# Kernel optimization log

Hardware: AMD Instinct MI355X
Metric: run time of the kernel (lower is better)

Reference implementation:

```python
import jax, jax.numpy as jnp
import numpy as np

B, DIN, N = 8, 256, 2048  # batch, input_dim (orig node_num), attention nodes (orig seq_len)


def setup_inputs() -> dict:
    key = jax.random.key(0)
    k1, k2, k3, k4 = jax.random.split(key, 4)
    x = jax.random.normal(k1, (B, DIN, N), jnp.float32)
    adj = jax.random.randint(k2, (N, N), 0, 2).astype(jnp.int32)  # binary adjacency
    W = jax.random.normal(k3, (DIN, DIN), jnp.float32) * 0.05      # Linear(D, D, bias=False), stored (out, in)
    a = jax.random.normal(k4, (3 * DIN,), jnp.float32) * 0.05      # Linear(3D, 1, bias=False)
    return {"x": x, "adj": adj, "W": W, "a": a}


def reference(x, adj, W, a):
    # x: (B, D, N) -> permute to (B, N, D); attention is over the N axis
    xt = jnp.transpose(x, (0, 2, 1))
    h = xt @ W.T                                   # (B, N, D)
    sim = jnp.einsum('bid,bjd->bij', h, h)         # (B, N, N) pairwise dot products
    n = adj.shape[0]
    # neighbor mask: adj nonzero, diagonal forced off (mask[:, i] = 0 in the loop)
    m = (adj != 0) & (~jnp.eye(n, dtype=bool))
    # context: the torch loop's weighted_h is independent of its k axis, so
    # context[b, k, i, d] == C[b, i, d] = sum_j m[i,j] * sim[b,i,j] * h[b,j,d]
    C = jnp.einsum('bij,bjd->bid', jnp.where(m[None, :, :], sim, 0.0), h)  # (B, N, D)
    d = h.shape[-1]
    a1, a2, a3 = a[:d], a[d:2 * d], a[2 * d:]
    # a([h_i, h_j, C_j]) = a1.h_i + a2.h_j + a3.C_j  (concat never materialized)
    s_i = h @ a1                                   # (B, N)
    s_j = h @ a2 + C @ a3                          # (B, N)
    scores = jax.nn.leaky_relu(s_i[:, :, None] + s_j[:, None, :], negative_slope=0.2)
    scores = jnp.where(adj[None, :, :] == 0, jnp.float32(-9e15), scores)
    return jax.nn.softmax(scores, axis=-1)         # (B, N, N)
```

## Files before the change

kernel.cpp:

```cpp
#include <hip/hip_runtime.h>
#include <hip/hip_bf16.h>
#include <math.h>

#define Bq   8
#define DINq 256
#define Nq   2048

typedef __attribute__((ext_vector_type(8))) short bf16x8v;
typedef __attribute__((ext_vector_type(4))) float f32x4v;

__device__ __forceinline__ unsigned short f2bf(float f) {
  union { float f; unsigned u; } v; v.f = f;
  unsigned r = v.u + 0x7fffu + ((v.u >> 16) & 1u);
  return (unsigned short)(r >> 16);
}
__device__ __forceinline__ float bf2f(unsigned short h) {
  union { unsigned u; float f; } v; v.u = ((unsigned)h) << 16;
  return v.f;
}

__device__ __forceinline__ void gld_lds16(const void* g, void* l) {
  __builtin_amdgcn_global_load_lds(
      (const __attribute__((address_space(1))) unsigned int*)g,
      (__attribute__((address_space(3))) unsigned int*)l, 16, 0, 0);
}

__global__ void k_prep(const float* __restrict__ W, const float* __restrict__ a,
                       float* __restrict__ w123) {
  int k = threadIdx.x;
  float s1 = 0.f, s2 = 0.f, s3 = 0.f;
  for (int d = 0; d < DINq; ++d) {
    float w = W[d * DINq + k];
    s1 += w * a[d];
    s2 += w * a[DINq + d];
    s3 += w * a[2 * DINq + d];
  }
  w123[k] = s1; w123[DINq + k] = s2; w123[2 * DINq + k] = s3;
}

__global__ void k_transposeW(const float* __restrict__ W, float* __restrict__ WT) {
  int d = blockIdx.x, k = threadIdx.x;
  WT[(size_t)k * DINq + d] = W[(size_t)d * DINq + k];
}

__global__ __launch_bounds__(256, 2) void k_hX(const float* __restrict__ x,
                     const float* __restrict__ WT, const float* __restrict__ w123,
                     unsigned short* __restrict__ Xhi, unsigned short* __restrict__ Xlo,
                     float* __restrict__ tA, float* __restrict__ siA,
                     float* __restrict__ sbA) {
  __shared__ float xs[64][32];
  __shared__ float ws[64][128];
  __shared__ float wls[3][256];
  __shared__ float Pd[3][16][32];
  __shared__ float Tt[32];
  const int tid = threadIdx.x;
  const int iq = tid & 15;
  const int dg = tid >> 4;
  const int i0 = blockIdx.x * 32;
  const int b = blockIdx.y;

  for (int n = tid; n < 768; n += 256) ((float*)wls)[n] = w123[n];

  float p1[2] = {0.f, 0.f}, p2[2] = {0.f, 0.f}, p3[2] = {0.f, 0.f};

#pragma unroll
  for (int dh = 0; dh < 2; ++dh) {
    float acc[2][8];
#pragma unroll
    for (int aa = 0; aa < 2; ++aa)
#pragma unroll
      for (int cc = 0; cc < 8; ++cc) acc[aa][cc] = 0.f;

    for (int kc = 0; kc < 4; ++kc) {
      __syncthreads();
#pragma unroll
      for (int n = 0; n < 8; ++n) {
        int idx = n * 256 + tid;
        int kk = idx >> 5, ii = idx & 31;
        xs[kk][ii] = x[((size_t)b * DINq + kc * 64 + kk) * Nq + i0 + ii];
      }
#pragma unroll
      for (int n = 0; n < 8; ++n) {
        int idx = n * 256 + tid;
        int kk = idx >> 5, c4 = (idx & 31) * 4;
        *(f32x4v*)&ws[kk][c4] =
            *(const f32x4v*)&WT[(size_t)(kc * 64 + kk) * DINq + dh * 128 + c4];
      }
      __syncthreads();
#pragma unroll 4
      for (int kk = 0; kk < 64; ++kk) {
        float xv0 = xs[kk][iq * 2], xv1 = xs[kk][iq * 2 + 1];
        f32x4v w0 = *(const f32x4v*)&ws[kk][dg * 8];
        f32x4v w1 = *(const f32x4v*)&ws[kk][dg * 8 + 4];
#pragma unroll
        for (int cc = 0; cc < 4; ++cc) {
          acc[0][cc]     += xv0 * w0[cc];
          acc[0][cc + 4] += xv0 * w1[cc];
          acc[1][cc]     += xv1 * w0[cc];
          acc[1][cc + 4] += xv1 * w1[cc];
        }
      }
      if (dh == 0) {
#pragma unroll
        for (int kap = 0; kap < 4; ++kap) {
          int kk = dg * 4 + kap;
          float xv0 = xs[kk][iq * 2], xv1 = xs[kk][iq * 2 + 1];
          float w3 = wls[2][kc * 64 + kk];
          float w1v = wls[0][kc * 64 + kk], w2v = wls[1][kc * 64 + kk];
          p3[0] += xv0 * w3;  p3[1] += xv1 * w3;
          p1[0] += xv0 * w1v; p1[1] += xv1 * w1v;
          p2[0] += xv0 * w2v; p2[1] += xv1 * w2v;
        }
      }
    }

    if (dh == 0) {
#pragma unroll
      for (int aa = 0; aa < 2; ++aa) {
        Pd[0][dg][iq * 2 + aa] = p1[aa];
        Pd[1][dg][iq * 2 + aa] = p2[aa];
        Pd[2][dg][iq * 2 + aa] = p3[aa];
      }
      __syncthreads();
      if (tid < 32) {
        float t = 0.f, s1 = 0.f, s2 = 0.f;
#pragma unroll
        for (int g = 0; g < 16; ++g) {
          s1 += Pd[0][g][tid]; s2 += Pd[1][g][tid]; t += Pd[2][g][tid];
        }
        Tt[tid] = t;
        tA[(size_t)b * Nq + i0 + tid] = t;
        siA[(size_t)b * Nq + i0 + tid] = s1;
        sbA[(size_t)b * Nq + i0 + tid] = s2;
      }
      __syncthreads();
    }

    const float tv0 = Tt[iq * 2], tv1 = Tt[iq * 2 + 1];
#pragma unroll
    for (int cc = 0; cc < 8; ++cc) {
      int d = dh * 128 + dg * 8 + cc;
      float X0 = tv0 * acc[0][cc];
      float X1 = tv1 * acc[1][cc];
      unsigned short h0 = f2bf(X0), h1 = f2bf(X1);
      unsigned short l0 = f2bf(X0 - bf2f(h0)), l1 = f2bf(X1 - bf2f(h1));
      size_t xoff = ((size_t)b * DINq + d) * Nq + i0 + iq * 2;
      *(ushort2*)&Xhi[xoff] = make_ushort2(h0, h1);
      *(ushort2*)&Xlo[xoff] = make_ushort2(l0, l1);
    }
  }
}

__global__ void k_mask(const int* __restrict__ adj, unsigned short* __restrict__ Mb,
                       unsigned* __restrict__ bm) {
  int wg = blockIdx.x * 256 + threadIdx.x;
  int i = wg >> 6, w = wg & 63, j0 = w * 32;
  const int4* ap = (const int4*)&adj[(size_t)i * Nq + j0];
  unsigned bits = 0;
  unsigned short mv[32];
#pragma unroll
  for (int q = 0; q < 8; ++q) {
    int4 a = ap[q];
    int av[4] = {a.x, a.y, a.z, a.w};
#pragma unroll
    for (int e = 0; e < 4; ++e) {
      int j = j0 + q * 4 + e;
      bool nz = (av[e] != 0);
      if (nz) bits |= 1u << (q * 4 + e);
      mv[q * 4 + e] = (nz && j != i) ? (unsigned short)0x3F80 : (unsigned short)0;
    }
  }
  ushort4* mp = (ushort4*)&Mb[(size_t)i * Nq + j0];
#pragma unroll
  for (int q = 0; q < 8; ++q)
    mp[q] = make_ushort4(mv[q * 4], mv[q * 4 + 1], mv[q * 4 + 2], mv[q * 4 + 3]);
  bm[wg] = bits;
}

__global__ __launch_bounds__(256, 2) void k_gemm(const unsigned short* __restrict__ Mb,
                                                 const unsigned short* __restrict__ Xhi,
                                                 const unsigned short* __restrict__ Xlo,
                                                 float* __restrict__ sjp) {
  __shared__ __align__(16) unsigned short As[3][256 * 32];
  __shared__ __align__(16) unsigned short Bs[3][128 * 32];
  const int tid = threadIdx.x;
  const int lane = tid & 63;
  const int wave = tid >> 6;
  const int wm = wave >> 1, wc = wave & 1;
  const int wg = blockIdx.x;
  const int lin = (wg & 7) * 64 + (wg >> 3);
  const int mt = lin >> 6;
  const int rem = lin & 63;
  const int ks = rem >> 5;
  const int z = (rem >> 4) & 1;
  const int ct = rem & 15;
  const int i0 = mt * 256, c0 = ct * 128, kbase = ks * 1024;
  const unsigned short* __restrict__ Xp = z ? Xlo : Xhi;
  const int r15 = lane & 15, kg = lane >> 4;
  const int kb = (kg * 16) ^ ((r15 & 3) << 4);

  f32x4v acc[8][4];
#pragma unroll
  for (int m = 0; m < 8; ++m)
#pragma unroll
    for (int n = 0; n < 4; ++n) acc[m][n] = (f32x4v)0.f;

  auto STAGE = [&](int buf, int t) {
    const int k0 = kbase + t * 32;
#pragma unroll
    for (int l = 0; l < 4; ++l) {
      const int pc = l * 256 + tid;
      const int row = pc >> 2, q = pc & 3;
      const int kc = 8 * (q ^ (row & 3));
      gld_lds16(&Mb[(size_t)(i0 + row) * Nq + k0 + kc], &As[buf][pc * 8]);
    }
#pragma unroll
    for (int l = 0; l < 2; ++l) {
      const int pc = l * 256 + tid;
      const int row = pc >> 2, q = pc & 3;
      const int kc = 8 * (q ^ (row & 3));
      gld_lds16(&Xp[(size_t)(c0 + row) * Nq + k0 + kc], &Bs[buf][pc * 8]);
    }
  };

  constexpr int NT = 32;
  STAGE(0, 0);
  STAGE(1, 1);
  int cb = 0, sb2 = 2;
  for (int t = 0; t < NT; ++t) {
    if (t + 1 < NT) {
      asm volatile("s_waitcnt vmcnt(6)" ::: "memory");
    } else {
      asm volatile("s_waitcnt vmcnt(0)" ::: "memory");
    }
    __builtin_amdgcn_sched_barrier(0);
    __builtin_amdgcn_s_barrier();
    __builtin_amdgcn_sched_barrier(0);
    if (t + 2 < NT) STAGE(sb2, t + 2);

    const char* Ab = (const char*)&As[cb][0];
    const char* Bb = (const char*)&Bs[cb][0];
    bf16x8v af[8], bf[4];
#pragma unroll
    for (int m = 0; m < 8; ++m)
      af[m] = *(const bf16x8v*)(Ab + (wm * 128 + m * 16 + r15) * 64 + kb);
#pragma unroll
    for (int n = 0; n < 4; ++n)
      bf[n] = *(const bf16x8v*)(Bb + (wc * 64 + n * 16 + r15) * 64 + kb);
    __builtin_amdgcn_s_setprio(1);
#pragma unroll
    for (int m = 0; m < 8; ++m)
#pragma unroll
      for (int n = 0; n < 4; ++n)
        acc[m][n] = __builtin_amdgcn_mfma_f32_16x16x32_bf16(af[m], bf[n], acc[m][n], 0, 0, 0);
    __builtin_amdgcn_s_setprio(0);
    cb = (cb == 2) ? 0 : cb + 1;
    sb2 = (sb2 == 2) ? 0 : sb2 + 1;
  }

  const int b = c0 >> 8;
  const int re = (lane >> 4) * 4, ce = lane & 15;
  float s[8][4];
#pragma unroll
  for (int m = 0; m < 8; ++m)
#pragma unroll
    for (int r = 0; r < 4; ++r) s[m][r] = 0.f;
#pragma unroll
  for (int n = 0; n < 4; ++n) {
    const size_t xrow = (size_t)(c0 + wc * 64 + n * 16 + ce) * Nq;
#pragma unroll
    for (int m = 0; m < 8; ++m) {
      const size_t ib = xrow + i0 + wm * 128 + m * 16 + re;
      ushort4 xh = *(const ushort4*)&Xhi[ib];
      ushort4 xl = *(const ushort4*)&Xlo[ib];
      s[m][0] += acc[m][n][0] * (bf2f(xh.x) + bf2f(xl.x));
      s[m][1] += acc[m][n][1] * (bf2f(xh.y) + bf2f(xl.y));
      s[m][2] += acc[m][n][2] * (bf2f(xh.z) + bf2f(xl.z));
      s[m][3] += acc[m][n][3] * (bf2f(xh.w) + bf2f(xl.w));
    }
  }
#pragma unroll
  for (int o = 1; o < 16; o <<= 1) {
#pragma unroll
    for (int m = 0; m < 8; ++m)
#pragma unroll
      for (int r = 0; r < 4; ++r) s[m][r] += __shfl_xor(s[m][r], o, 64);
  }
  if (ce == 0) {
    const int slice = ks * 8 + z * 4 + (ct & 1) * 2 + wc;
    float* sp = sjp + ((size_t)slice * Bq + b) * Nq;
#pragma unroll
    for (int m = 0; m < 8; ++m)
#pragma unroll
      for (int r = 0; r < 4; ++r)
        sp[i0 + wm * 128 + m * 16 + re + r] = s[m][r];
  }
}

__global__ void k_sjsum(const float* __restrict__ sbA, const float* __restrict__ tA,
                        const float* __restrict__ sjp, float* __restrict__ sjvA) {
  int idx = blockIdx.x * 256 + threadIdx.x;
  float s = 0.f;
#pragma unroll
  for (int sl = 0; sl < 16; ++sl) s += sjp[(size_t)sl * Bq * Nq + idx];
  sjvA[idx] = sbA[idx] + s / tA[idx];
}

__global__ void k_softmax(const unsigned* __restrict__ bm, const float* __restrict__ siA,
                          const float* __restrict__ sjvA, float* __restrict__ out) {
  const int b = blockIdx.y, i = blockIdx.x, tid = threadIdx.x;
  const float siv = siA[(size_t)b * Nq + i];
  const unsigned* brow = bm + (size_t)i * 64;
  const float* sjb = sjvA + (size_t)b * Nq;
  const int bit = tid & 31;
  float sc[8];
  float mx = -3.0e38f;
#pragma unroll
  for (int s = 0; s < 8; ++s) {
    int j = s * 256 + tid;
    float v = siv + sjb[j];
    v = v > 0.f ? v : 0.2f * v;
    unsigned wv = brow[j >> 5];
    v = ((wv >> bit) & 1u) ? v : -9.0e15f;
    sc[s] = v;
    mx = fmaxf(mx, v);
  }
#pragma unroll
  for (int o = 32; o >= 1; o >>= 1) mx = fmaxf(mx, __shfl_xor(mx, o, 64));
  __shared__ float redm[4], reds[4];
  const int wave = tid >> 6, lane = tid & 63;
  if (lane == 0) redm[wave] = mx;
  __syncthreads();
  mx = fmaxf(fmaxf(redm[0], redm[1]), fmaxf(redm[2], redm[3]));
  float sum = 0.f, ex[8];
#pragma unroll
  for (int s = 0; s < 8; ++s) { ex[s] = expf(sc[s] - mx); sum += ex[s]; }
#pragma unroll
  for (int o = 32; o >= 1; o >>= 1) sum += __shfl_xor(sum, o, 64);
  if (lane == 0) reds[wave] = sum;
  __syncthreads();
  sum = reds[0] + reds[1] + reds[2] + reds[3];
  float inv = 1.f / sum;
  float* orow = out + ((size_t)b * Nq + i) * Nq;
#pragma unroll
  for (int s = 0; s < 8; ++s) orow[s * 256 + tid] = ex[s] * inv;
}

extern "C" void kernel_launch(void* const* d_in, const int* in_sizes, int n_in,
                              void* d_out, int out_size, void* d_ws, size_t ws_size,
                              hipStream_t stream) {
  const float* x = (const float*)d_in[0];
  const int* adj = (const int*)d_in[1];
  const float* W = (const float*)d_in[2];
  const float* a = (const float*)d_in[3];
  float* out = (float*)d_out;

  char* ws = (char*)d_ws;
  size_t off = 0;
  auto alloc = [&](size_t bytes) -> void* {
    void* p = ws + off;
    off += (bytes + 255) & ~(size_t)255;
    return p;
  };
  float* w123 = (float*)alloc(3 * DINq * sizeof(float));
  float* WT = (float*)alloc((size_t)DINq * DINq * sizeof(float));
  float* tA = (float*)alloc((size_t)Bq * Nq * sizeof(float));
  float* siA = (float*)alloc((size_t)Bq * Nq * sizeof(float));
  float* sbA = (float*)alloc((size_t)Bq * Nq * sizeof(float));
  float* sjvA = (float*)alloc((size_t)Bq * Nq * sizeof(float));
  float* sjp = (float*)alloc((size_t)16 * Bq * Nq * sizeof(float));
  unsigned short* Xhi = (unsigned short*)alloc((size_t)Nq * Nq * 2);
  unsigned short* Xlo = (unsigned short*)alloc((size_t)Nq * Nq * 2);
  unsigned short* Mb = (unsigned short*)alloc((size_t)Nq * Nq * 2);
  unsigned* bm = (unsigned*)alloc((size_t)Nq * 64 * sizeof(unsigned));

  k_prep<<<dim3(1), dim3(256), 0, stream>>>(W, a, w123);
  k_transposeW<<<dim3(DINq), dim3(DINq), 0, stream>>>(W, WT);
  k_hX<<<dim3(Nq / 32, Bq), dim3(256), 0, stream>>>(x, WT, w123, Xhi, Xlo, tA, siA, sbA);
  k_mask<<<dim3(Nq * 64 / 256), dim3(256), 0, stream>>>(adj, Mb, bm);
  k_gemm<<<dim3(512), dim3(256), 0, stream>>>(Mb, Xhi, Xlo, sjp);
  k_sjsum<<<dim3(Bq * Nq / 256), dim3(256), 0, stream>>>(sbA, tA, sjp, sjvA);
  k_softmax<<<dim3(Nq, Bq), dim3(256), 0, stream>>>(bm, siA, sjvA, out);
}
```

Before: 148.9 us.

## Move h projection to bf16 split-precision MFMA GEMM with transposed scaled inputs

Replaces the FP32 scalar-FMA k_hX kernel with three stages: a dot-product kernel for t/si/sb, a kernel that scales x by t and writes transposed hi/lo bf16 copies, and an MFMA GEMM (hi*hi + lo*hi + hi*lo, three K segments) against a hi/lo bf16 split of W. It also changes the LDS swizzle pattern in the main GEMM to a row-pair XOR. The aim is to run the projection on matrix cores instead of vector ALUs. In exchange it adds two launches and round-trips larger intermediate buffers (yhi/ylo) through global memory, and the split-bf16 scheme drops the lo*lo term.

```diff
diff --git a/kernel.cpp b/kernel.cpp
--- a/kernel.cpp
+++ b/kernel.cpp
@@ -38,116 +38,189 @@
   w123[k] = s1; w123[DINq + k] = s2; w123[2 * DINq + k] = s3;
 }
 
-__global__ void k_transposeW(const float* __restrict__ W, float* __restrict__ WT) {
-  int d = blockIdx.x, k = threadIdx.x;
-  WT[(size_t)k * DINq + d] = W[(size_t)d * DINq + k];
-}
-
-__global__ __launch_bounds__(256, 2) void k_hX(const float* __restrict__ x,
-                     const float* __restrict__ WT, const float* __restrict__ w123,
-                     unsigned short* __restrict__ Xhi, unsigned short* __restrict__ Xlo,
-                     float* __restrict__ tA, float* __restrict__ siA,
-                     float* __restrict__ sbA) {
-  __shared__ float xs[64][32];
-  __shared__ float ws[64][128];
-  __shared__ float wls[3][256];
-  __shared__ float Pd[3][16][32];
-  __shared__ float Tt[32];
+__global__ void k_wsplit(const float* __restrict__ W, unsigned short* __restrict__ Whi,
+                         unsigned short* __restrict__ Wlo) {
+  int idx = blockIdx.x * 256 + threadIdx.x;
+  float w = W[idx];
+  unsigned short h = f2bf(w);
+  Whi[idx] = h;
+  Wlo[idx] = f2bf(w - bf2f(h));
+}
+
+__global__ void k_tsisb(const float* __restrict__ x, const float* __restrict__ w123,
+                        float* __restrict__ tA, float* __restrict__ siA,
+                        float* __restrict__ sbA) {
+  int b = blockIdx.y;
+  int il = threadIdx.x & 63;
+  int i = blockIdx.x * 64 + il;
+  int ks = (threadIdx.x >> 6) * 64;
+  float a1 = 0.f, a2 = 0.f, a3 = 0.f;
+  for (int k = ks; k < ks + 64; ++k) {
+    float xv = x[((size_t)b * DINq + k) * Nq + i];
+    a1 += xv * w123[k];
+    a2 += xv * w123[DINq + k];
+    a3 += xv * w123[2 * DINq + k];
+  }
+  __shared__ float r1[256], r2[256], r3[256];
+  r1[threadIdx.x] = a1; r2[threadIdx.x] = a2; r3[threadIdx.x] = a3;
+  __syncthreads();
+  if (threadIdx.x < 64) {
+    int l = threadIdx.x;
+    float v1 = r1[l] + r1[64 + l] + r1[128 + l] + r1[192 + l];
+    float v2 = r2[l] + r2[64 + l] + r2[128 + l] + r2[192 + l];
+    float v3 = r3[l] + r3[64 + l] + r3[128 + l] + r3[192 + l];
+    int ii = blockIdx.x * 64 + l;
+    siA[(size_t)b * Nq + ii] = v1;
+    sbA[(size_t)b * Nq + ii] = v2;
+    tA[(size_t)b * Nq + ii] = v3;
+  }
+}
+
+__global__ __launch_bounds__(256) void k_yT(const float* __restrict__ x,
+                    const float* __restrict__ tA, unsigned short* __restrict__ yhi,
+                    unsigned short* __restrict__ ylo) {
+  __shared__ unsigned lds[64][129];
+  __shared__ float tl[64];
   const int tid = threadIdx.x;
-  const int iq = tid & 15;
-  const int dg = tid >> 4;
-  const int i0 = blockIdx.x * 32;
+  const int i0 = blockIdx.x * 64;
   const int b = blockIdx.y;
-
-  for (int n = tid; n < 768; n += 256) ((float*)wls)[n] = w123[n];
-
-  float p1[2] = {0.f, 0.f}, p2[2] = {0.f, 0.f}, p3[2] = {0.f, 0.f};
-
-#pragma unroll
-  for (int dh = 0; dh < 2; ++dh) {
-    float acc[2][8];
-#pragma unroll
-    for (int aa = 0; aa < 2; ++aa)
-#pragma unroll
-      for (int cc = 0; cc < 8; ++cc) acc[aa][cc] = 0.f;
-
-    for (int kc = 0; kc < 4; ++kc) {
-      __syncthreads();
-#pragma unroll
-      for (int n = 0; n < 8; ++n) {
-        int idx = n * 256 + tid;
-        int kk = idx >> 5, ii = idx & 31;
-        xs[kk][ii] = x[((size_t)b * DINq + kc * 64 + kk) * Nq + i0 + ii];
+  if (tid < 64) tl[tid] = tA[(size_t)b * Nq + i0 + tid];
+  for (int kh = 0; kh < 2; ++kh) {
+    __syncthreads();
+#pragma unroll 4
+    for (int n = 0; n < 32; ++n) {
+      int idx = n * 256 + tid;
+      int k = idx >> 6, i = idx & 63;
+      float xv = x[((size_t)b * DINq + kh * 128 + k) * Nq + i0 + i];
+      float yv = tl[i] * xv;
+      unsigned short h = f2bf(yv);
+      unsigned short l = f2bf(yv - bf2f(h));
+      lds[i][k] = (unsigned)h | ((unsigned)l << 16);
+    }
+    __syncthreads();
+    const int i = tid >> 2, kq = (tid & 3) * 32;
+    size_t base = ((size_t)b * Nq + i0 + i) * DINq + kh * 128 + kq;
+#pragma unroll
+    for (int g = 0; g < 8; ++g) {
+      unsigned short hh[4], ll[4];
+#pragma unroll
+      for (int e = 0; e < 4; ++e) {
+        unsigned v = lds[i][kq + g * 4 + e];
+        hh[e] = (unsigned short)(v & 0xffff);
+        ll[e] = (unsigned short)(v >> 16);
       }
-#pragma unroll
-      for (int n = 0; n < 8; ++n) {
-        int idx = n * 256 + tid;
-        int kk = idx >> 5, c4 = (idx & 31) * 4;
-        *(f32x4v*)&ws[kk][c4] =
-            *(const f32x4v*)&WT[(size_t)(kc * 64 + kk) * DINq + dh * 128 + c4];
+      *(ushort4*)&yhi[base + g * 4] = make_ushort4(hh[0], hh[1], hh[2], hh[3]);
+      *(ushort4*)&ylo[base + g * 4] = make_ushort4(ll[0], ll[1], ll[2], ll[3]);
+    }
+  }
+}
+
+__global__ __launch_bounds__(256, 2) void k_hX2(const unsigned short* __restrict__ yhi,
+                    const unsigned short* __restrict__ ylo,
+                    const unsigned short* __restrict__ Whi,
+                    const unsigned short* __restrict__ Wlo,
+                    unsigned short* __restrict__ Xhi, unsigned short* __restrict__ Xlo) {
+  __shared__ __align__(16) unsigned short As[3][64 * 32];
+  __shared__ __align__(16) unsigned short Bs[3][128 * 32];
+  __shared__ unsigned xout[128][65];
+  const int tid = threadIdx.x;
+  const int lane = tid & 63;
+  const int wc = tid >> 6;
+  const int wg = blockIdx.x;
+  const int b = wg >> 6;
+  const int rem = wg & 63;
+  const int it = rem >> 1, dh = rem & 1;
+  const int r15 = lane & 15, kg = lane >> 4;
+  const int kb = 16 * (kg ^ ((r15 >> 1) & 3));
+
+  f32x4v acc[4][2];
+#pragma unroll
+  for (int m = 0; m < 4; ++m)
+#pragma unroll
+    for (int n = 0; n < 2; ++n) acc[m][n] = (f32x4v)0.f;
+
+  auto STAGE = [&](int buf, int t) {
+    const int seg = t >> 3;
+    const int k0 = (t & 7) * 32;
+    const unsigned short* ys = (seg == 1) ? ylo : yhi;
+    const unsigned short* wsrc = (seg == 2) ? Wlo : Whi;
+    {
+      const int row = tid >> 2, q = tid & 3;
+      const int kc = 8 * (q ^ ((row >> 1) & 3));
+      gld_lds16(&ys[((size_t)b * Nq + it * 64 + row) * DINq + k0 + kc], &As[buf][tid * 8]);
+    }
+#pragma unroll
+    for (int l = 0; l < 2; ++l) {
+      const int pc = l * 256 + tid;
+      const int row = pc >> 2, q = pc & 3;
+      const int kc = 8 * (q ^ ((row >> 1) & 3));
+      gld_lds16(&wsrc[(size_t)(dh * 128 + row) * DINq + k0 + kc], &Bs[buf][pc * 8]);
+    }
+  };
+
+  constexpr int NT = 24;
+  STAGE(0, 0);
+  STAGE(1, 1);
+  int cb = 0, sb2 = 2;
+  for (int t = 0; t < NT; ++t) {
+    if (t + 1 < NT) {
+      asm volatile("s_waitcnt vmcnt(3)" ::: "memory");
+    } else {
+      asm volatile("s_waitcnt vmcnt(0)" ::: "memory");
+    }
+    __builtin_amdgcn_sched_barrier(0);
+    __builtin_amdgcn_s_barrier();
+    __builtin_amdgcn_sched_barrier(0);
+    if (t + 2 < NT) STAGE(sb2, t + 2);
+
+    const char* Ab = (const char*)&As[cb][0];
+    const char* Bb = (const char*)&Bs[cb][0];
+    bf16x8v af[4], bf[2];
+#pragma unroll
+    for (int m = 0; m < 4; ++m)
+      af[m] = *(const bf16x8v*)(Ab + (m * 16 + r15) * 64 + kb);
+#pragma unroll
+    for (int n = 0; n < 2; ++n)
+      bf[n] = *(const bf16x8v*)(Bb + (wc * 32 + n * 16 + r15) * 64 + kb);
+    __builtin_amdgcn_s_setprio(1);
+#pragma unroll
+    for (int m = 0; m < 4; ++m)
+#pragma unroll
+      for (int n = 0; n < 2; ++n)
+        acc[m][n] = __builtin_amdgcn_mfma_f32_16x16x32_bf16(af[m], bf[n], acc[m][n], 0, 0, 0);
+    __builtin_amdgcn_s_setprio(0);
+    cb = (cb == 2) ? 0 : cb + 1;
+    sb2 = (sb2 == 2) ? 0 : sb2 + 1;
+  }
+
+  const int re = (lane >> 4) * 4, ce = lane & 15;
+#pragma unroll
+  for (int m = 0; m < 4; ++m)
+#pragma unroll
+    for (int n = 0; n < 2; ++n) {
+      const int dl = wc * 32 + n * 16 + ce;
+#pragma unroll
+      for (int r = 0; r < 4; ++r) {
+        float Xv = acc[m][n][r];
+        unsigned short h = f2bf(Xv);
+        unsigned short l = f2bf(Xv - bf2f(h));
+        xout[dl][m * 16 + re + r] = (unsigned)h | ((unsigned)l << 16);
       }
-      __syncthreads();
-#pragma unroll 4
-      for (int kk = 0; kk < 64; ++kk) {
-        float xv0 = xs[kk][iq * 2], xv1 = xs[kk][iq * 2 + 1];
-        f32x4v w0 = *(const f32x4v*)&ws[kk][dg * 8];
-        f32x4v w1 = *(const f32x4v*)&ws[kk][dg * 8 + 4];
-#pragma unroll
-        for (int cc = 0; cc < 4; ++cc) {
-          acc[0][cc]     += xv0 * w0[cc];
-          acc[0][cc + 4] += xv0 * w1[cc];
-          acc[1][cc]     += xv1 * w0[cc];
-          acc[1][cc + 4] += xv1 * w1[cc];
-        }
-      }
-      if (dh == 0) {
-#pragma unroll
-        for (int kap = 0; kap < 4; ++kap) {
-          int kk = dg * 4 + kap;
-          float xv0 = xs[kk][iq * 2], xv1 = xs[kk][iq * 2 + 1];
-          float w3 = wls[2][kc * 64 + kk];
-          float w1v = wls[0][kc * 64 + kk], w2v = wls[1][kc * 64 + kk];
-          p3[0] += xv0 * w3;  p3[1] += xv1 * w3;
-          p1[0] += xv0 * w1v; p1[1] += xv1 * w1v;
-          p2[0] += xv0 * w2v; p2[1] += xv1 * w2v;
-        }
-      }
-    }
-
-    if (dh == 0) {
-#pragma unroll
-      for (int aa = 0; aa < 2; ++aa) {
-        Pd[0][dg][iq * 2 + aa] = p1[aa];
-        Pd[1][dg][iq * 2 + aa] = p2[aa];
-        Pd[2][dg][iq * 2 + aa] = p3[aa];
-      }
-      __syncthreads();
-      if (tid < 32) {
-        float t = 0.f, s1 = 0.f, s2 = 0.f;
-#pragma unroll
-        for (int g = 0; g < 16; ++g) {
-          s1 += Pd[0][g][tid]; s2 += Pd[1][g][tid]; t += Pd[2][g][tid];
-        }
-        Tt[tid] = t;
-        tA[(size_t)b * Nq + i0 + tid] = t;
-        siA[(size_t)b * Nq + i0 + tid] = s1;
-        sbA[(size_t)b * Nq + i0 + tid] = s2;
-      }
-      __syncthreads();
-    }
-
-    const float tv0 = Tt[iq * 2], tv1 = Tt[iq * 2 + 1];
-#pragma unroll
-    for (int cc = 0; cc < 8; ++cc) {
-      int d = dh * 128 + dg * 8 + cc;
-      float X0 = tv0 * acc[0][cc];
-      float X1 = tv1 * acc[1][cc];
-      unsigned short h0 = f2bf(X0), h1 = f2bf(X1);
-      unsigned short l0 = f2bf(X0 - bf2f(h0)), l1 = f2bf(X1 - bf2f(h1));
-      size_t xoff = ((size_t)b * DINq + d) * Nq + i0 + iq * 2;
-      *(ushort2*)&Xhi[xoff] = make_ushort2(h0, h1);
-      *(ushort2*)&Xlo[xoff] = make_ushort2(l0, l1);
-    }
+    }
+  __syncthreads();
+  const int d = tid >> 1, ih = (tid & 1) * 32;
+  size_t base = ((size_t)b * DINq + dh * 128 + d) * Nq + it * 64 + ih;
+#pragma unroll
+  for (int g = 0; g < 8; ++g) {
+    unsigned short hh[4], ll[4];
+#pragma unroll
+    for (int e = 0; e < 4; ++e) {
+      unsigned v = xout[d][ih + g * 4 + e];
+      hh[e] = (unsigned short)(v & 0xffff);
+      ll[e] = (unsigned short)(v >> 16);
+    }
+    *(ushort4*)&Xhi[base + g * 4] = make_ushort4(hh[0], hh[1], hh[2], hh[3]);
+    *(ushort4*)&Xlo[base + g * 4] = make_ushort4(ll[0], ll[1], ll[2], ll[3]);
   }
 }
 
@@ -197,7 +270,7 @@
   const int i0 = mt * 256, c0 = ct * 128, kbase = ks * 1024;
   const unsigned short* __restrict__ Xp = z ? Xlo : Xhi;
   const int r15 = lane & 15, kg = lane >> 4;
-  const int kb = (kg * 16) ^ ((r15 & 3) << 4);
+  const int kb = 16 * (kg ^ ((r15 >> 1) & 3));
 
   f32x4v acc[8][4];
 #pragma unroll
@@ -211,14 +284,14 @@
     for (int l = 0; l < 4; ++l) {
       const int pc = l * 256 + tid;
       const int row = pc >> 2, q = pc & 3;
-      const int kc = 8 * (q ^ (row & 3));
+      const int kc = 8 * (q ^ ((row >> 1) & 3));
       gld_lds16(&Mb[(size_t)(i0 + row) * Nq + k0 + kc], &As[buf][pc * 8]);
     }
 #pragma unroll
     for (int l = 0; l < 2; ++l) {
       const int pc = l * 256 + tid;
       const int row = pc >> 2, q = pc & 3;
-      const int kc = 8 * (q ^ (row & 3));
+      const int kc = 8 * (q ^ ((row >> 1) & 3));
       gld_lds16(&Xp[(size_t)(c0 + row) * Nq + k0 + kc], &Bs[buf][pc * 8]);
     }
   };
@@ -363,21 +436,26 @@
     return p;
   };
   float* w123 = (float*)alloc(3 * DINq * sizeof(float));
-  float* WT = (float*)alloc((size_t)DINq * DINq * sizeof(float));
   float* tA = (float*)alloc((size_t)Bq * Nq * sizeof(float));
   float* siA = (float*)alloc((size_t)Bq * Nq * sizeof(float));
   float* sbA = (float*)alloc((size_t)Bq * Nq * sizeof(float));
   float* sjvA = (float*)alloc((size_t)Bq * Nq * sizeof(float));
   float* sjp = (float*)alloc((size_t)16 * Bq * Nq * sizeof(float));
+  unsigned short* Whi = (unsigned short*)alloc((size_t)DINq * DINq * 2);
+  unsigned short* Wlo = (unsigned short*)alloc((size_t)DINq * DINq * 2);
+  unsigned short* yhi = (unsigned short*)alloc((size_t)Bq * Nq * DINq * 2);
+  unsigned short* ylo = (unsigned short*)alloc((size_t)Bq * Nq * DINq * 2);
   unsigned short* Xhi = (unsigned short*)alloc((size_t)Nq * Nq * 2);
   unsigned short* Xlo = (unsigned short*)alloc((size_t)Nq * Nq * 2);
   unsigned short* Mb = (unsigned short*)alloc((size_t)Nq * Nq * 2);
   unsigned* bm = (unsigned*)alloc((size_t)Nq * 64 * sizeof(unsigned));
 
   k_prep<<<dim3(1), dim3(256), 0, stream>>>(W, a, w123);
-  k_transposeW<<<dim3(DINq), dim3(DINq), 0, stream>>>(W, WT);
-  k_hX<<<dim3(Nq / 32, Bq), dim3(256), 0, stream>>>(x, WT, w123, Xhi, Xlo, tA, siA, sbA);
+  k_wsplit<<<dim3(DINq * DINq / 256), dim3(256), 0, stream>>>(W, Whi, Wlo);
+  k_tsisb<<<dim3(Nq / 64, Bq), dim3(256), 0, stream>>>(x, w123, tA, siA, sbA);
+  k_yT<<<dim3(Nq / 64, Bq), dim3(256), 0, stream>>>(x, tA, yhi, ylo);
   k_mask<<<dim3(Nq * 64 / 256), dim3(256), 0, stream>>>(adj, Mb, bm);
+  k_hX2<<<dim3(512), dim3(256), 0, stream>>>(yhi, ylo, Whi, Wlo, Xhi, Xlo);
   k_gemm<<<dim3(512), dim3(256), 0, stream>>>(Mb, Xhi, Xlo, sjp);
   k_sjsum<<<dim3(Bq * Nq / 256), dim3(256), 0, stream>>>(sbA, tA, sjp, sjvA);
   k_softmax<<<dim3(Nq, Bq), dim3(256), 0, stream>>>(bm, siA, sjvA, out);
```

Measured after the change: 155.5 us. +4.4%, slower.
